# Performance work log

Hardware: AMD Instinct MI355X
Metric: run time of the kernel (lower is better)

The kernel has to match this reference:

```python
import jax, jax.numpy as jnp
import numpy as np

KE = 14.3996
ALPHA = 0.3
CUTOFF = 10.0
K_MAX = 6
N_ATOMS = 100000
N_PAIRS = 6400000
N_MOL = 64


def _generate_kvecs():
    kr = np.arange(0, K_MAX + 1, dtype=np.float32)
    kr = np.concatenate([kr, -kr[1:]])
    # cartesian product of (kr, kr, kr)
    g = np.stack(np.meshgrid(kr, kr, kr, indexing='ij'), axis=-1).reshape(-1, 3)
    norm = (g ** 2).sum(axis=1)
    mask = (norm <= K_MAX ** 2 + 2) & (norm != 0)
    return jnp.asarray(g[mask])  # [1020, 3]


def setup_inputs() -> dict:
    key = jax.random.key(0)
    k1, k2, k3, k4, k5, k6, k7 = jax.random.split(key, 7)
    partial_charges = jax.random.normal(k1, (N_ATOMS, 1), dtype=jnp.float32)
    # pair displacement vectors; scale so typical |r_ij| ~ 3-6 A, avoids d ~ 0
    Rij = jax.random.normal(k2, (N_PAIRS, 3), dtype=jnp.float32) * 3.0 + 1.0
    R = jax.random.uniform(k3, (N_ATOMS, 3), dtype=jnp.float32) * 20.0
    # orthorhombic-ish invertible cells: diag(~20) + small perturbation
    cell = jnp.eye(3, dtype=jnp.float32)[None] * 20.0 \
        + jax.random.uniform(k4, (N_MOL, 3, 3), dtype=jnp.float32) * 0.1
    idx_m = jnp.sort(jax.random.randint(k5, (N_ATOMS,), 0, N_MOL)).astype(jnp.int64)
    idx_i = jax.random.randint(k6, (N_PAIRS,), 0, N_ATOMS).astype(jnp.int64)
    idx_j = jax.random.randint(k7, (N_PAIRS,), 0, N_ATOMS).astype(jnp.int64)
    kvecs = _generate_kvecs()
    return {"partial_charges": partial_charges, "Rij": Rij, "R": R, "cell": cell,
            "kvecs": kvecs, "idx_m": idx_m, "idx_i": idx_i, "idx_j": idx_j}


def reference(partial_charges, Rij, R, cell, kvecs, idx_m, idx_i, idx_j):
    q = partial_charges.squeeze(-1)                      # [A]
    d_ij = jnp.linalg.norm(Rij, axis=1)                  # [P]
    sqrt_a = jnp.sqrt(jnp.float32(ALPHA))

    # ---- real space: gather q, erfc-screened pair potential, double scatter ----
    f_r = jax.scipy.special.erfc(sqrt_a * d_ij) / d_ij
    f_r_cut = jax.scipy.special.erfc(sqrt_a * CUTOFF) / CUTOFF
    pot_ij = q[idx_i] * q[idx_j] * (f_r - f_r_cut)
    pot_ij = jnp.where(d_ij <= CUTOFF, pot_ij, jnp.zeros_like(pot_ij))
    y_atom = jax.ops.segment_sum(pot_ij, idx_i, num_segments=N_ATOMS)
    y_real = 0.5 * KE * jax.ops.segment_sum(y_atom, idx_m, num_segments=N_MOL)

    # ---- reciprocal space ----
    two_pi = 2.0 * jnp.float32(np.pi)
    recip_box = two_pi * jnp.transpose(jnp.linalg.inv(cell), (0, 2, 1))  # [M,3,3]
    v_box = jnp.abs(jnp.linalg.det(cell))                                # [M]
    prefactor = two_pi / v_box
    kv = jnp.einsum('kd,mde->mke', kvecs, recip_box)     # [M,K,3]
    k_sq = jnp.sum(kv ** 2, axis=2)                      # [M,K]
    q_gauss = jnp.exp(-0.25 * k_sq / ALPHA)              # [M,K]
    # per-atom phase: gather per-molecule k-vectors, dot with positions
    kdp = jnp.einsum('akd,ad->ak', kv[idx_m], R)         # [A,K]
    q_real = jax.ops.segment_sum(q[:, None] * jnp.cos(kdp), idx_m, num_segments=N_MOL)
    q_imag = jax.ops.segment_sum(q[:, None] * jnp.sin(kdp), idx_m, num_segments=N_MOL)
    q_dens = q_real ** 2 + q_imag ** 2                   # [M,K]
    y_ewald = prefactor * jnp.sum(q_dens * q_gauss / k_sq, axis=1)
    self_int = jnp.sqrt(ALPHA / np.pi) * jax.ops.segment_sum(q ** 2, idx_m, num_segments=N_MOL)
    y_recip = KE * (y_ewald - self_int)

    return y_real + y_recip                              # [M]
```

## Files before the change

kernel.cpp:

```cpp
#include <hip/hip_runtime.h>
#include <math.h>

#define KE_C     14.3996f
#define ALPHA_C  0.3f
#define CUTOFF_C 10.0f
#define TWO_PI_C 6.283185307179586f
#define INV_2PI  0.15915494309189535f
#define ASPL     32
#define NK2      512
#define NREAL    2048

typedef float vfloat4 __attribute__((ext_vector_type(4)));
typedef int   vint4   __attribute__((ext_vector_type(4)));

__device__ __forceinline__ float fast_erfc(float x) {
    float t = __builtin_amdgcn_rcpf(fmaf(0.3275911f, x, 1.0f));
    float p = fmaf(t, 1.061405429f, -1.453152027f);
    p = fmaf(t, p, 1.421413741f);
    p = fmaf(t, p, -0.284496736f);
    p = fmaf(t, p, 0.254829592f);
    return t * p * __expf(-x * x);
}

__device__ __forceinline__ void sincos_rev(float x, float* s, float* c) {
    float f = __builtin_amdgcn_fractf(x);
    *s = __builtin_amdgcn_sinf(f);
    *c = __builtin_amdgcn_cosf(f);
}

__global__ __launch_bounds__(64) void k_cell(const float* __restrict__ cell,
                                             float* __restrict__ RB,
                                             float* __restrict__ VB, int nmol) {
    int m = blockIdx.x * blockDim.x + threadIdx.x;
    if (m >= nmol) return;
    const float* c = cell + m * 9;
    float a00 = c[0], a01 = c[1], a02 = c[2];
    float a10 = c[3], a11 = c[4], a12 = c[5];
    float a20 = c[6], a21 = c[7], a22 = c[8];
    float det = a00 * (a11 * a22 - a12 * a21)
              - a01 * (a10 * a22 - a12 * a20)
              + a02 * (a10 * a21 - a11 * a20);
    float id = 1.0f / det;
    float inv00 = (a11 * a22 - a12 * a21) * id;
    float inv01 = (a02 * a21 - a01 * a22) * id;
    float inv02 = (a01 * a12 - a02 * a11) * id;
    float inv10 = (a12 * a20 - a10 * a22) * id;
    float inv11 = (a00 * a22 - a02 * a20) * id;
    float inv12 = (a02 * a10 - a00 * a12) * id;
    float inv20 = (a10 * a21 - a11 * a20) * id;
    float inv21 = (a01 * a20 - a00 * a21) * id;
    float inv22 = (a00 * a11 - a01 * a10) * id;
    float* rb = RB + m * 9;
    rb[0] = TWO_PI_C * inv00; rb[1] = TWO_PI_C * inv10; rb[2] = TWO_PI_C * inv20;
    rb[3] = TWO_PI_C * inv01; rb[4] = TWO_PI_C * inv11; rb[5] = TWO_PI_C * inv21;
    rb[6] = TWO_PI_C * inv02; rb[7] = TWO_PI_C * inv12; rb[8] = TWO_PI_C * inv22;
    VB[m] = fabsf(det);
}

__global__ __launch_bounds__(128) void k_bounds(const int* __restrict__ idx_m,
                                                int* __restrict__ bounds,
                                                int natoms, int nmol) {
    int m = threadIdx.x;
    if (m > nmol) return;
    int lo = 0, hi = natoms;
    while (lo < hi) {
        int mid = (lo + hi) >> 1;
        if (idx_m[mid] < m) lo = mid + 1; else hi = mid;
    }
    bounds[m] = lo;
}

__global__ __launch_bounds__(256) void k_khalf(const float* __restrict__ kvecs,
                                               float4* __restrict__ KH,
                                               int* __restrict__ cnt, int nk) {
    int k = blockIdx.x * 256 + threadIdx.x;
    if (k >= nk) return;
    float gx = kvecs[3 * k], gy = kvecs[3 * k + 1], gz = kvecs[3 * k + 2];
    bool pos = (gx > 0.5f) ||
               (fabsf(gx) < 0.5f && (gy > 0.5f ||
                (fabsf(gy) < 0.5f && gz > 0.5f)));
    if (pos) {
        int s = atomicAdd(cnt, 1);
        KH[s] = make_float4(gx, gy, gz, 0.0f);
    }
}

__global__ __launch_bounds__(256) void k_atoms(const float* __restrict__ R,
                                               const float* __restrict__ q,
                                               const int* __restrict__ idx_m,
                                               const float* __restrict__ RB,
                                               float4* __restrict__ S4,
                                               unsigned int* __restrict__ QP,
                                               float* __restrict__ SI, int natoms) {
    __shared__ float si[64];
    int tid = threadIdx.x;
    if (tid < 64) si[tid] = 0.0f;
    __syncthreads();
    int a = blockIdx.x * 256 + tid;
    if (a < natoms) {
        int m = idx_m[a];
        float r0 = R[3 * a], r1 = R[3 * a + 1], r2 = R[3 * a + 2];
        const float* rb = RB + m * 9;
        float s0 = (rb[0] * r0 + rb[1] * r1 + rb[2] * r2) * INV_2PI;
        float s1 = (rb[3] * r0 + rb[4] * r1 + rb[5] * r2) * INV_2PI;
        float s2 = (rb[6] * r0 + rb[7] * r1 + rb[8] * r2) * INV_2PI;
        float qa = q[a];
        S4[a] = make_float4(s0, s1, s2, qa);
        QP[a] = (__float_as_uint(qa) & ~63u) | (unsigned int)(m & 63);
        atomicAdd(&si[m & 63], qa * qa);
    }
    __syncthreads();
    if (tid < 64) atomicAdd(&SI[tid], si[tid]);
}

__global__ __launch_bounds__(256) void k_main(const float4* __restrict__ S4,
                                              const float4* __restrict__ KH,
                                              const int* __restrict__ bounds,
                                              float* __restrict__ QR,
                                              float* __restrict__ QI, int nrecip,
                                              const float* __restrict__ Rij,
                                              const int* __restrict__ idx_i,
                                              const int* __restrict__ idx_j,
                                              const unsigned int* __restrict__ QP,
                                              float* __restrict__ YRpad, int npairs) {
    __shared__ float acc[4][64];
    int tid = threadIdx.x;
    int bid = blockIdx.x;

    if (bid < nrecip) {
        int m  = bid / ASPL;
        int ac = bid % ASPL;
        int s0 = bounds[m], s1 = bounds[m + 1];
        int per = (s1 - s0 + ASPL - 1) / ASPL;
        int a0 = s0 + ac * per;
        int a1 = min(a0 + per, s1);
        float4 g0 = KH[tid];
        float4 g1 = KH[tid + 256];
        float qr0 = 0.f, qi0 = 0.f, qr1 = 0.f, qi1 = 0.f;
#pragma unroll 4
        for (int t = a0; t < a1; ++t) {
            float4 s = S4[t];
            float ph0 = fmaf(g0.x, s.x, fmaf(g0.y, s.y, g0.z * s.z));
            float ph1 = fmaf(g1.x, s.x, fmaf(g1.y, s.y, g1.z * s.z));
            float sn0, cs0, sn1, cs1;
            sincos_rev(ph0, &sn0, &cs0);
            sincos_rev(ph1, &sn1, &cs1);
            qr0 = fmaf(s.w, cs0, qr0);
            qi0 = fmaf(s.w, sn0, qi0);
            qr1 = fmaf(s.w, cs1, qr1);
            qi1 = fmaf(s.w, sn1, qi1);
        }
        atomicAdd(&QR[m * NK2 + tid], qr0);
        atomicAdd(&QI[m * NK2 + tid], qi0);
        atomicAdd(&QR[m * NK2 + tid + 256], qr1);
        atomicAdd(&QI[m * NK2 + tid + 256], qi1);
    } else {
        int wave = tid >> 6;
        ((float*)acc)[tid] = 0.0f;
        __syncthreads();
        const float sqa = 0.5477225575051661f;
        const float frcut = fast_erfc(sqa * CUTOFF_C) / CUTOFF_C;
        int nchunk = npairs >> 2;
        int stride = NREAL * 256;
        for (int c = (bid - nrecip) * 256 + tid; c < nchunk; c += stride) {
            int p = c << 2;
            vint4 ii = *(const vint4*)(idx_i + p);
            vint4 jj = *(const vint4*)(idx_j + p);
            const vfloat4* r4 = (const vfloat4*)(Rij + 3 * p);
            vfloat4 A = r4[0], B = r4[1], C = r4[2];
            unsigned int ui0 = QP[ii.x], ui1 = QP[ii.y], ui2 = QP[ii.z], ui3 = QP[ii.w];
            unsigned int uj0 = QP[jj.x], uj1 = QP[jj.y], uj2 = QP[jj.z], uj3 = QP[jj.w];
#define PAIR(xx, yy, zz, ui, uj)                                              \
            {                                                                 \
                float d2 = fmaf(xx, xx, fmaf(yy, yy, (zz) * (zz)));           \
                float rd = __builtin_amdgcn_rsqf(d2);                         \
                float d = d2 * rd;                                            \
                float f = fast_erfc(sqa * d) * rd - frcut;                    \
                f = (d2 <= CUTOFF_C * CUTOFF_C) ? f : 0.0f;                   \
                float qi_ = __uint_as_float((ui) & ~63u);                     \
                float qj_ = __uint_as_float((uj) & ~63u);                     \
                atomicAdd(&acc[wave][(ui) & 63u], qi_ * qj_ * f);             \
            }
            PAIR(A.x, A.y, A.z, ui0, uj0)
            PAIR(A.w, B.x, B.y, ui1, uj1)
            PAIR(B.z, B.w, C.x, ui2, uj2)
            PAIR(C.y, C.z, C.w, ui3, uj3)
#undef PAIR
        }
        if (bid == nrecip && tid == 0) {
            for (int p = (npairs >> 2) << 2; p < npairs; ++p) {
                float x = Rij[3 * p], y = Rij[3 * p + 1], z = Rij[3 * p + 2];
                float d2 = fmaf(x, x, fmaf(y, y, z * z));
                if (d2 <= CUTOFF_C * CUTOFF_C) {
                    float rd = __builtin_amdgcn_rsqf(d2);
                    float d = d2 * rd;
                    unsigned int ui = QP[idx_i[p]], uj = QP[idx_j[p]];
                    float qi_ = __uint_as_float(ui & ~63u);
                    float qj_ = __uint_as_float(uj & ~63u);
                    atomicAdd(&acc[0][ui & 63u],
                              qi_ * qj_ * (fast_erfc(sqa * d) * rd - frcut));
                }
            }
        }
        __syncthreads();
        if (tid < 64) {
            float v = acc[0][tid] + acc[1][tid] + acc[2][tid] + acc[3][tid];
            atomicAdd(&YRpad[tid * 16], v);
        }
    }
}

__global__ __launch_bounds__(256) void k_final(const float4* __restrict__ KH,
                                               const int* __restrict__ cnt,
                                               const float* __restrict__ RB,
                                               const float* __restrict__ VB,
                                               const float* __restrict__ QR,
                                               const float* __restrict__ QI,
                                               const float* __restrict__ YRpad,
                                               const float* __restrict__ SI,
                                               float* __restrict__ out) {
    int m = blockIdx.x;
    int tid = threadIdx.x;
    __shared__ float rb[9];
    __shared__ float wsum[4];
    if (tid < 9) rb[tid] = RB[m * 9 + tid];
    __syncthreads();
    int nhalf = cnt[0];
    float acc = 0.0f;
    for (int k = tid; k < nhalf; k += 256) {
        float4 g = KH[k];
        float kv0 = g.x * rb[0] + g.y * rb[3] + g.z * rb[6];
        float kv1 = g.x * rb[1] + g.y * rb[4] + g.z * rb[7];
        float kv2 = g.x * rb[2] + g.y * rb[5] + g.z * rb[8];
        float ksq = kv0 * kv0 + kv1 * kv1 + kv2 * kv2;
        float qr = QR[m * NK2 + k], qi = QI[m * NK2 + k];
        acc += (qr * qr + qi * qi) * __expf(-0.25f / ALPHA_C * ksq) / ksq;
    }
#pragma unroll
    for (int off = 32; off > 0; off >>= 1) acc += __shfl_down(acc, off, 64);
    if ((tid & 63) == 0) wsum[tid >> 6] = acc;
    __syncthreads();
    if (tid == 0) {
        float s = 2.0f * (wsum[0] + wsum[1] + wsum[2] + wsum[3]);
        float pref = TWO_PI_C / VB[m];
        float self_c = sqrtf(ALPHA_C / 3.14159265358979323846f);
        out[m] = 0.5f * KE_C * YRpad[m * 16] + KE_C * (pref * s - self_c * SI[m]);
    }
}

extern "C" void kernel_launch(void* const* d_in, const int* in_sizes, int n_in,
                              void* d_out, int out_size, void* d_ws, size_t ws_size,
                              hipStream_t stream) {
    const float* q     = (const float*)d_in[0];
    const float* Rij   = (const float*)d_in[1];
    const float* R     = (const float*)d_in[2];
    const float* cell  = (const float*)d_in[3];
    const float* kvecs = (const float*)d_in[4];
    const int*   idx_m = (const int*)d_in[5];
    const int*   idx_i = (const int*)d_in[6];
    const int*   idx_j = (const int*)d_in[7];

    int natoms = in_sizes[0];
    int npairs = in_sizes[1] / 3;
    int nmol   = in_sizes[3] / 9;
    int nk     = in_sizes[4] / 3;
    float* out = (float*)d_out;

    float*  W      = (float*)d_ws;
    float*  RB     = W;
    float*  VB     = RB + 576;
    int*    bounds = (int*)(VB + 64);
    float4* S4     = (float4*)(W + 720);
    unsigned int* QP = (unsigned int*)(W + 720 + 4 * (size_t)natoms);
    size_t  zoff   = 720 + 5 * (size_t)natoms;
    zoff = (zoff + 3) & ~(size_t)3;
    float4* KH     = (float4*)(W + zoff);
    float*  QR     = W + zoff + 4 * NK2;
    float*  QI     = QR + (size_t)nmol * NK2;
    float*  SI     = QI + (size_t)nmol * NK2;
    float*  YRpad  = SI + 64;
    int*    cnt    = (int*)(YRpad + 64 * 16);
    size_t zero_bytes = (4 * NK2 + (size_t)2 * nmol * NK2 + 64 + 64 * 16 + 4) * sizeof(float);
    (void)hipMemsetAsync(KH, 0, zero_bytes, stream);

    int nrecip = nmol * ASPL;
    k_cell  <<<1, 64, 0, stream>>>(cell, RB, VB, nmol);
    k_bounds<<<1, 128, 0, stream>>>(idx_m, bounds, natoms, nmol);
    k_khalf <<<(nk + 255) / 256, 256, 0, stream>>>(kvecs, KH, cnt, nk);
    k_atoms <<<(natoms + 255) / 256, 256, 0, stream>>>(R, q, idx_m, RB, S4, QP, SI, natoms);
    k_main  <<<nrecip + NREAL, 256, 0, stream>>>(S4, KH, bounds, QR, QI, nrecip,
                                                 Rij, idx_i, idx_j, QP, YRpad, npairs);
    k_final <<<nmol, 256, 0, stream>>>(KH, cnt, RB, VB, QR, QI, YRpad, SI, out);
}
```

Baseline: 247.1 us.

## Merge setup kernels, interleave recip/real blocks, software-pipeline pair loads

Folds the cell-inverse, bounds, k-half and per-atom kernels into one launch, recomputing the 3x3 inverse per atom and in the final kernel so no RB/VB buffers or extra launches are needed. In the main kernel, reciprocal and real-space blocks are interleaved by block index so both kinds of work are spread across CUs early. The real-space loop prefetches the next chunk's indices and displacements before processing the current one to hide memory latency. The trade-off is redundant inverse computation and higher register pressure from the prefetch buffers.

Measured after the change: 270.2 us. 1.09x slower.

```diff
diff --git a/kernel.cpp b/kernel.cpp
--- a/kernel.cpp
+++ b/kernel.cpp
@@ -5,7 +5,6 @@
 #define ALPHA_C  0.3f
 #define CUTOFF_C 10.0f
 #define TWO_PI_C 6.283185307179586f
-#define INV_2PI  0.15915494309189535f
 #define ASPL     32
 #define NK2      512
 #define NREAL    2048
@@ -28,12 +27,7 @@
     *c = __builtin_amdgcn_cosf(f);
 }
 
-__global__ __launch_bounds__(64) void k_cell(const float* __restrict__ cell,
-                                             float* __restrict__ RB,
-                                             float* __restrict__ VB, int nmol) {
-    int m = blockIdx.x * blockDim.x + threadIdx.x;
-    if (m >= nmol) return;
-    const float* c = cell + m * 9;
+__device__ __forceinline__ float inv3x3(const float* c, float* inv) {
     float a00 = c[0], a01 = c[1], a02 = c[2];
     float a10 = c[3], a11 = c[4], a12 = c[5];
     float a20 = c[6], a21 = c[7], a22 = c[8];
@@ -41,76 +35,74 @@
               - a01 * (a10 * a22 - a12 * a20)
               + a02 * (a10 * a21 - a11 * a20);
     float id = 1.0f / det;
-    float inv00 = (a11 * a22 - a12 * a21) * id;
-    float inv01 = (a02 * a21 - a01 * a22) * id;
-    float inv02 = (a01 * a12 - a02 * a11) * id;
-    float inv10 = (a12 * a20 - a10 * a22) * id;
-    float inv11 = (a00 * a22 - a02 * a20) * id;
-    float inv12 = (a02 * a10 - a00 * a12) * id;
-    float inv20 = (a10 * a21 - a11 * a20) * id;
-    float inv21 = (a01 * a20 - a00 * a21) * id;
-    float inv22 = (a00 * a11 - a01 * a10) * id;
-    float* rb = RB + m * 9;
-    rb[0] = TWO_PI_C * inv00; rb[1] = TWO_PI_C * inv10; rb[2] = TWO_PI_C * inv20;
-    rb[3] = TWO_PI_C * inv01; rb[4] = TWO_PI_C * inv11; rb[5] = TWO_PI_C * inv21;
-    rb[6] = TWO_PI_C * inv02; rb[7] = TWO_PI_C * inv12; rb[8] = TWO_PI_C * inv22;
-    VB[m] = fabsf(det);
-}
-
-__global__ __launch_bounds__(128) void k_bounds(const int* __restrict__ idx_m,
-                                                int* __restrict__ bounds,
-                                                int natoms, int nmol) {
-    int m = threadIdx.x;
-    if (m > nmol) return;
-    int lo = 0, hi = natoms;
-    while (lo < hi) {
-        int mid = (lo + hi) >> 1;
-        if (idx_m[mid] < m) lo = mid + 1; else hi = mid;
-    }
-    bounds[m] = lo;
-}
-
-__global__ __launch_bounds__(256) void k_khalf(const float* __restrict__ kvecs,
-                                               float4* __restrict__ KH,
-                                               int* __restrict__ cnt, int nk) {
-    int k = blockIdx.x * 256 + threadIdx.x;
-    if (k >= nk) return;
-    float gx = kvecs[3 * k], gy = kvecs[3 * k + 1], gz = kvecs[3 * k + 2];
-    bool pos = (gx > 0.5f) ||
-               (fabsf(gx) < 0.5f && (gy > 0.5f ||
-                (fabsf(gy) < 0.5f && gz > 0.5f)));
-    if (pos) {
-        int s = atomicAdd(cnt, 1);
-        KH[s] = make_float4(gx, gy, gz, 0.0f);
-    }
-}
-
-__global__ __launch_bounds__(256) void k_atoms(const float* __restrict__ R,
+    inv[0] = (a11 * a22 - a12 * a21) * id;
+    inv[1] = (a02 * a21 - a01 * a22) * id;
+    inv[2] = (a01 * a12 - a02 * a11) * id;
+    inv[3] = (a12 * a20 - a10 * a22) * id;
+    inv[4] = (a00 * a22 - a02 * a20) * id;
+    inv[5] = (a02 * a10 - a00 * a12) * id;
+    inv[6] = (a10 * a21 - a11 * a20) * id;
+    inv[7] = (a01 * a20 - a00 * a21) * id;
+    inv[8] = (a00 * a11 - a01 * a10) * id;
+    return det;
+}
+
+__global__ __launch_bounds__(256) void k_setup(const float* __restrict__ R,
                                                const float* __restrict__ q,
                                                const int* __restrict__ idx_m,
-                                               const float* __restrict__ RB,
+                                               const float* __restrict__ cell,
+                                               const float* __restrict__ kvecs,
                                                float4* __restrict__ S4,
                                                unsigned int* __restrict__ QP,
-                                               float* __restrict__ SI, int natoms) {
-    __shared__ float si[64];
+                                               float* __restrict__ SI,
+                                               int* __restrict__ bounds,
+                                               float4* __restrict__ KH,
+                                               int* __restrict__ cnt,
+                                               int natoms, int nmol, int nk, int NA) {
+    int bid = blockIdx.x;
     int tid = threadIdx.x;
-    if (tid < 64) si[tid] = 0.0f;
-    __syncthreads();
-    int a = blockIdx.x * 256 + tid;
-    if (a < natoms) {
-        int m = idx_m[a];
-        float r0 = R[3 * a], r1 = R[3 * a + 1], r2 = R[3 * a + 2];
-        const float* rb = RB + m * 9;
-        float s0 = (rb[0] * r0 + rb[1] * r1 + rb[2] * r2) * INV_2PI;
-        float s1 = (rb[3] * r0 + rb[4] * r1 + rb[5] * r2) * INV_2PI;
-        float s2 = (rb[6] * r0 + rb[7] * r1 + rb[8] * r2) * INV_2PI;
-        float qa = q[a];
-        S4[a] = make_float4(s0, s1, s2, qa);
-        QP[a] = (__float_as_uint(qa) & ~63u) | (unsigned int)(m & 63);
-        atomicAdd(&si[m & 63], qa * qa);
-    }
-    __syncthreads();
-    if (tid < 64) atomicAdd(&SI[tid], si[tid]);
+    if (bid < NA) {
+        __shared__ float si[64];
+        if (tid < 64) si[tid] = 0.0f;
+        __syncthreads();
+        int a = bid * 256 + tid;
+        if (a < natoms) {
+            int m = idx_m[a];
+            float inv[9];
+            inv3x3(cell + m * 9, inv);
+            float r0 = R[3 * a], r1 = R[3 * a + 1], r2 = R[3 * a + 2];
+            float s0 = inv[0] * r0 + inv[3] * r1 + inv[6] * r2;
+            float s1 = inv[1] * r0 + inv[4] * r1 + inv[7] * r2;
+            float s2 = inv[2] * r0 + inv[5] * r1 + inv[8] * r2;
+            float qa = q[a];
+            S4[a] = make_float4(s0, s1, s2, qa);
+            QP[a] = (__float_as_uint(qa) & ~63u) | (unsigned int)(m & 63);
+            atomicAdd(&si[m & 63], qa * qa);
+        }
+        __syncthreads();
+        if (tid < 64) atomicAdd(&SI[tid], si[tid]);
+    } else if (bid == NA) {
+        int m = tid;
+        if (m <= nmol) {
+            int lo = 0, hi = natoms;
+            while (lo < hi) {
+                int mid = (lo + hi) >> 1;
+                if (idx_m[mid] < m) lo = mid + 1; else hi = mid;
+            }
+            bounds[m] = lo;
+        }
+    } else {
+        for (int k = tid; k < nk; k += 256) {
+            float gx = kvecs[3 * k], gy = kvecs[3 * k + 1], gz = kvecs[3 * k + 2];
+            bool pos = (gx > 0.5f) ||
+                       (fabsf(gx) < 0.5f && (gy > 0.5f ||
+                        (fabsf(gy) < 0.5f && gz > 0.5f)));
+            if (pos) {
+                int s = atomicAdd(cnt, 1);
+                KH[s] = make_float4(gx, gy, gz, 0.0f);
+            }
+        }
+    }
 }
 
 __global__ __launch_bounds__(256) void k_main(const float4* __restrict__ S4,
@@ -127,9 +119,12 @@
     int tid = threadIdx.x;
     int bid = blockIdx.x;
 
-    if (bid < nrecip) {
-        int m  = bid / ASPL;
-        int ac = bid % ASPL;
+    bool recip = (bid < 2 * nrecip) && (bid & 1);
+    int idx = (bid < 2 * nrecip) ? (bid >> 1) : (bid - nrecip);
+
+    if (recip) {
+        int m  = idx / ASPL;
+        int ac = idx % ASPL;
         int s0 = bounds[m], s1 = bounds[m + 1];
         int per = (s1 - s0 + ASPL - 1) / ASPL;
         int a0 = s0 + ac * per;
@@ -162,12 +157,25 @@
         const float frcut = fast_erfc(sqa * CUTOFF_C) / CUTOFF_C;
         int nchunk = npairs >> 2;
         int stride = NREAL * 256;
-        for (int c = (bid - nrecip) * 256 + tid; c < nchunk; c += stride) {
+        int c = idx * 256 + tid;
+        vint4 ii, jj; vfloat4 A, B, C;
+        if (c < nchunk) {
             int p = c << 2;
-            vint4 ii = *(const vint4*)(idx_i + p);
-            vint4 jj = *(const vint4*)(idx_j + p);
+            ii = *(const vint4*)(idx_i + p);
+            jj = *(const vint4*)(idx_j + p);
             const vfloat4* r4 = (const vfloat4*)(Rij + 3 * p);
-            vfloat4 A = r4[0], B = r4[1], C = r4[2];
+            A = r4[0]; B = r4[1]; C = r4[2];
+        }
+        while (c < nchunk) {
+            int cn = c + stride;
+            vint4 ii2, jj2; vfloat4 A2, B2, C2;
+            if (cn < nchunk) {
+                int p = cn << 2;
+                ii2 = *(const vint4*)(idx_i + p);
+                jj2 = *(const vint4*)(idx_j + p);
+                const vfloat4* r4 = (const vfloat4*)(Rij + 3 * p);
+                A2 = r4[0]; B2 = r4[1]; C2 = r4[2];
+            }
             unsigned int ui0 = QP[ii.x], ui1 = QP[ii.y], ui2 = QP[ii.z], ui3 = QP[ii.w];
             unsigned int uj0 = QP[jj.x], uj1 = QP[jj.y], uj2 = QP[jj.z], uj3 = QP[jj.w];
 #define PAIR(xx, yy, zz, ui, uj)                                              \
@@ -186,8 +194,9 @@
             PAIR(B.z, B.w, C.x, ui2, uj2)
             PAIR(C.y, C.z, C.w, ui3, uj3)
 #undef PAIR
-        }
-        if (bid == nrecip && tid == 0) {
+            c = cn; ii = ii2; jj = jj2; A = A2; B = B2; C = C2;
+        }
+        if (bid == 0 && tid == 0) {
             for (int p = (npairs >> 2) << 2; p < npairs; ++p) {
                 float x = Rij[3 * p], y = Rij[3 * p + 1], z = Rij[3 * p + 2];
                 float d2 = fmaf(x, x, fmaf(y, y, z * z));
@@ -212,8 +221,7 @@
 
 __global__ __launch_bounds__(256) void k_final(const float4* __restrict__ KH,
                                                const int* __restrict__ cnt,
-                                               const float* __restrict__ RB,
-                                               const float* __restrict__ VB,
+                                               const float* __restrict__ cell,
                                                const float* __restrict__ QR,
                                                const float* __restrict__ QI,
                                                const float* __restrict__ YRpad,
@@ -221,17 +229,16 @@
                                                float* __restrict__ out) {
     int m = blockIdx.x;
     int tid = threadIdx.x;
-    __shared__ float rb[9];
     __shared__ float wsum[4];
-    if (tid < 9) rb[tid] = RB[m * 9 + tid];
-    __syncthreads();
+    float inv[9];
+    float det = inv3x3(cell + m * 9, inv);
     int nhalf = cnt[0];
     float acc = 0.0f;
     for (int k = tid; k < nhalf; k += 256) {
         float4 g = KH[k];
-        float kv0 = g.x * rb[0] + g.y * rb[3] + g.z * rb[6];
-        float kv1 = g.x * rb[1] + g.y * rb[4] + g.z * rb[7];
-        float kv2 = g.x * rb[2] + g.y * rb[5] + g.z * rb[8];
+        float kv0 = TWO_PI_C * (g.x * inv[0] + g.y * inv[1] + g.z * inv[2]);
+        float kv1 = TWO_PI_C * (g.x * inv[3] + g.y * inv[4] + g.z * inv[5]);
+        float kv2 = TWO_PI_C * (g.x * inv[6] + g.y * inv[7] + g.z * inv[8]);
         float ksq = kv0 * kv0 + kv1 * kv1 + kv2 * kv2;
         float qr = QR[m * NK2 + k], qi = QI[m * NK2 + k];
         acc += (qr * qr + qi * qi) * __expf(-0.25f / ALPHA_C * ksq) / ksq;
@@ -242,7 +249,7 @@
     __syncthreads();
     if (tid == 0) {
         float s = 2.0f * (wsum[0] + wsum[1] + wsum[2] + wsum[3]);
-        float pref = TWO_PI_C / VB[m];
+        float pref = TWO_PI_C / fabsf(det);
         float self_c = sqrtf(ALPHA_C / 3.14159265358979323846f);
         out[m] = 0.5f * KE_C * YRpad[m * 16] + KE_C * (pref * s - self_c * SI[m]);
     }
@@ -267,12 +274,10 @@
     float* out = (float*)d_out;
 
     float*  W      = (float*)d_ws;
-    float*  RB     = W;
-    float*  VB     = RB + 576;
-    int*    bounds = (int*)(VB + 64);
-    float4* S4     = (float4*)(W + 720);
-    unsigned int* QP = (unsigned int*)(W + 720 + 4 * (size_t)natoms);
-    size_t  zoff   = 720 + 5 * (size_t)natoms;
+    int*    bounds = (int*)W;
+    float4* S4     = (float4*)(W + 80);
+    unsigned int* QP = (unsigned int*)(W + 80 + 4 * (size_t)natoms);
+    size_t  zoff   = 80 + 5 * (size_t)natoms;
     zoff = (zoff + 3) & ~(size_t)3;
     float4* KH     = (float4*)(W + zoff);
     float*  QR     = W + zoff + 4 * NK2;
@@ -283,12 +288,11 @@
     size_t zero_bytes = (4 * NK2 + (size_t)2 * nmol * NK2 + 64 + 64 * 16 + 4) * sizeof(float);
     (void)hipMemsetAsync(KH, 0, zero_bytes, stream);
 
+    int NA = (natoms + 255) / 256;
     int nrecip = nmol * ASPL;
-    k_cell  <<<1, 64, 0, stream>>>(cell, RB, VB, nmol);
-    k_bounds<<<1, 128, 0, stream>>>(idx_m, bounds, natoms, nmol);
-    k_khalf <<<(nk + 255) / 256, 256, 0, stream>>>(kvecs, KH, cnt, nk);
-    k_atoms <<<(natoms + 255) / 256, 256, 0, stream>>>(R, q, idx_m, RB, S4, QP, SI, natoms);
-    k_main  <<<nrecip + NREAL, 256, 0, stream>>>(S4, KH, bounds, QR, QI, nrecip,
-                                                 Rij, idx_i, idx_j, QP, YRpad, npairs);
-    k_final <<<nmol, 256, 0, stream>>>(KH, cnt, RB, VB, QR, QI, YRpad, SI, out);
-}
+    k_setup<<<NA + 2, 256, 0, stream>>>(R, q, idx_m, cell, kvecs, S4, QP, SI,
+                                        bounds, KH, cnt, natoms, nmol, nk, NA);
+    k_main <<<nrecip + NREAL, 256, 0, stream>>>(S4, KH, bounds, QR, QI, nrecip,
+                                                Rij, idx_i, idx_j, QP, YRpad, npairs);
+    k_final<<<nmol, 256, 0, stream>>>(KH, cnt, cell, QR, QI, YRpad, SI, out);
+}
```
